# Optimization experiments

Hardware: AMD Instinct MI355X
Metric: run time of the kernel (lower is better)

## Reference

```python
import jax, jax.numpy as jnp
import numpy as np
from math import sqrt

T, B, V = 32, 16, 30000
D, DQKV = 300, 150
K, G = 10, 32            # top-K globals, grapharea_size neighbours each
S = 25000                # last_idx_senses (= SC rows)
EPS = 1e-8


def setup_inputs() -> dict:
    key = jax.random.key(0)
    ks = jax.random.split(key, 6)
    return {
        "predictions_globals": jax.random.normal(ks[0], (T, B, V), jnp.float32),
        "location_context": jax.random.normal(ks[1], (T, B, D), jnp.float32),
        "SC": jax.random.normal(ks[2], (S, D), jnp.float32),
        "Wq": jax.random.normal(ks[3], (D, DQKV), jnp.float32) / sqrt(D),
        "Wk": jax.random.normal(ks[4], (D, DQKV), jnp.float32) / sqrt(D),
        "neighbours_table": jax.random.randint(ks[5], (V, G), 0, S, jnp.int64),
    }


def reference(predictions_globals, location_context, SC, Wq, Wk, neighbours_table):
    # 1) per-sample top-K global selection (sort descending, take K indices)
    _, topk_idx = jax.lax.top_k(predictions_globals, K)          # [T,B,K]
    # 2) sense-neighbour lookup: K globals x G neighbours -> N = K*G senses
    neigh = neighbours_table[topk_idx].reshape(T, B, K * G)      # [T,B,N] int
    # 3) gather precomputed sense contexts
    senses_context = SC[neigh]                                   # [T,B,N,D]
    # 4) ComputeLogits: QK attention logits
    q = location_context @ Wq                                    # [T,B,dqkv]
    k = senses_context @ Wk                                      # [T,B,N,dqkv]
    logits = jnp.einsum("tbd,tbnd->tbn", q, k) / sqrt(DQKV)      # [T,B,N]
    # 5) softmax over neighbours, scatter into full sense distribution
    p = jax.nn.softmax(logits, axis=-1)                          # [T,B,N]
    base = jnp.full((T * B, S), EPS, dtype=p.dtype)
    rows = jnp.arange(T * B)[:, None]                            # [TB,1]
    senses_softmax = base.at[rows, neigh.reshape(T * B, -1)].set(p.reshape(T * B, -1))
    # 6) log-probabilities over all senses
    return jnp.log(senses_softmax)                               # [T*B, S]
```

## Files before the change

kernel.cpp:

```cpp
#include <hip/hip_runtime.h>
#include <math.h>

#define T_ 32
#define B_ 16
#define V_ 30000
#define V4 7500
#define D_ 300
#define DQKV_ 150
#define K_ 10
#define G_ 32
#define N_ 320
#define S_ 25000
#define S4 6250
#define SLICE 3125
#define QKP 304
#define NTS 1024
#define NTP 512
#define NTG 256
#define NTF 384
#define LCAP 4096
#define UTH 0xC0000000u

__device__ __forceinline__ unsigned umap(float f) {
    unsigned b = __float_as_uint(f);
    unsigned mask = (unsigned)(((int)b) >> 31);
    return b ^ (mask | 0x80000000u);
}
__device__ __forceinline__ bool better_u(unsigned au, int ai, unsigned bu, int bi) {
    return (au > bu) || (au == bu && ai < bi);
}

__global__ __launch_bounds__(NTS, 2) void scan_kernel(
    const float* __restrict__ pred, float* __restrict__ out,
    int* __restrict__ wstop)
{
    const int row = blockIdx.x, tid = threadIdx.x;
    const int lane = tid & 63, wave = tid >> 6;
    __shared__ unsigned lu[LCAP];
    __shared__ int      li[LCAP];
    __shared__ int      cnt;

    if (tid == 0) cnt = 0;
    __syncthreads();

    const float FILL = -18.420680743952367f;
    {
        float4 f4 = make_float4(FILL, FILL, FILL, FILL);
        float4* o4 = (float4*)(out + (size_t)row * S_);
        #pragma unroll
        for (int k = 0; k < 7; ++k) { int i = tid + k * NTS; if (i < S4) o4[i] = f4; }
    }

    {
        const float4* p4 = (const float4*)(pred + (size_t)row * V_);
        #pragma unroll
        for (int k = 0; k < 8; ++k) {
            int i = tid + k * NTS;
            if (i < V4) {
                float4 v = p4[i];
                unsigned u0 = umap(v.x), u1 = umap(v.y), u2 = umap(v.z), u3 = umap(v.w);
                int base = i * 4;
                if (u0 >= UTH) { int p = atomicAdd(&cnt, 1); if (p < LCAP) { lu[p] = u0; li[p] = base; } }
                if (u1 >= UTH) { int p = atomicAdd(&cnt, 1); if (p < LCAP) { lu[p] = u1; li[p] = base + 1; } }
                if (u2 >= UTH) { int p = atomicAdd(&cnt, 1); if (p < LCAP) { lu[p] = u2; li[p] = base + 2; } }
                if (u3 >= UTH) { int p = atomicAdd(&cnt, 1); if (p < LCAP) { lu[p] = u3; li[p] = base + 3; } }
            }
        }
    }
    __syncthreads();
    const int c = cnt;

    if (c >= K_ && c <= LCAP) {
        if (wave == 0) {
            for (int p = 0; p < K_; ++p) {
                unsigned bu = 0; int bi = 0x7fffffff;
                for (int s = lane; s < c; s += 64) {
                    unsigned uu = lu[s]; int ii = li[s];
                    if (better_u(uu, ii, bu, bi)) { bu = uu; bi = ii; }
                }
                #pragma unroll
                for (int off = 32; off; off >>= 1) {
                    unsigned ou = __shfl_xor(bu, off, 64);
                    int      oi = __shfl_xor(bi, off, 64);
                    if (better_u(ou, oi, bu, bi)) { bu = ou; bi = oi; }
                }
                if (lane == 0) wstop[row * K_ + p] = bi;
                for (int s = lane; s < c; s += 64)
                    if (li[s] == bi && lu[s] == bu) lu[s] = 0;
            }
        }
    } else {
        if (wave == 0) {
            unsigned tu[K_]; int tix[K_];
            #pragma unroll
            for (int s = 0; s < K_; ++s) { tu[s] = 0; tix[s] = 0x7fffffff; }
            const float* prow = pred + (size_t)row * V_;
            for (int i = lane; i < V_; i += 64) {
                unsigned u = umap(prow[i]);
                if (better_u(u, i, tu[K_-1], tix[K_-1])) {
                    tu[K_-1] = u; tix[K_-1] = i;
                    #pragma unroll
                    for (int s = K_-1; s > 0; --s)
                        if (better_u(tu[s], tix[s], tu[s-1], tix[s-1])) {
                            unsigned a = tu[s]; tu[s] = tu[s-1]; tu[s-1] = a;
                            int b2 = tix[s]; tix[s] = tix[s-1]; tix[s-1] = b2;
                        }
                }
            }
            for (int p = 0; p < K_; ++p) {
                unsigned bu = tu[0]; int bi = tix[0];
                #pragma unroll
                for (int s = 1; s < K_; ++s)
                    if (better_u(tu[s], tix[s], bu, bi)) { bu = tu[s]; bi = tix[s]; }
                #pragma unroll
                for (int off = 32; off; off >>= 1) {
                    unsigned ou = __shfl_xor(bu, off, 64);
                    int      oi = __shfl_xor(bi, off, 64);
                    if (better_u(ou, oi, bu, bi)) { bu = ou; bi = oi; }
                }
                if (lane == 0) wstop[row * K_ + p] = bi;
                #pragma unroll
                for (int s = 0; s < K_; ++s)
                    if (tix[s] == bi) tu[s] = 0;
            }
        }
    }
}

__global__ __launch_bounds__(NTP, 2) void prep_kernel(
    const float* __restrict__ lc, const float* __restrict__ Wq,
    const float* __restrict__ Wk, const int* __restrict__ nbt,
    const int* __restrict__ wstop,
    float* __restrict__ qkws, int* __restrict__ nidxws)
{
    const int row = blockIdx.x, tid = threadIdx.x;
    const int lane = tid & 63, wave = tid >> 6;
    __shared__ int   topg[K_];
    __shared__ __align__(16) float lcs[D_];
    __shared__ float qpart[2][DQKV_];

    if (tid < K_) topg[tid] = wstop[row * K_ + tid];
    if (tid >= 64 && tid < 64 + D_ / 4)
        ((float4*)lcs)[tid - 64] = ((const float4*)(lc + (size_t)row * D_))[tid - 64];
    __syncthreads();

    if (tid < N_) nidxws[(size_t)row * N_ + tid] = nbt[topg[tid >> 5] * G_ + (tid & 31)];

    if (tid < 2 * DQKV_) {
        int h = tid / DQKV_;
        int j = tid - h * DQKV_;
        int d0 = h * 150;
        const float* wp = Wq + (size_t)d0 * DQKV_ + j;
        float a0 = 0.f, a1 = 0.f;
        #pragma unroll 5
        for (int dd = 0; dd < 150; dd += 2) {
            a0 += lcs[d0 + dd]     * wp[(size_t)dd * DQKV_];
            a1 += lcs[d0 + dd + 1] * wp[(size_t)(dd + 1) * DQKV_];
        }
        qpart[h][j] = a0 + a1;
    }
    __syncthreads();

    {
        float qv0 = qpart[0][lane] + qpart[1][lane];
        float qv1 = qpart[0][64 + lane] + qpart[1][64 + lane];
        float qv2 = (lane < 22) ? (qpart[0][128 + lane] + qpart[1][128 + lane]) : 0.f;
        for (int d = wave; d < D_; d += 8) {
            const float* wr = Wk + (size_t)d * DQKV_;
            float w0 = wr[lane];
            float w1 = wr[64 + lane];
            float w2 = (lane < 22) ? wr[128 + lane] : 0.f;
            float p = w0 * qv0 + w1 * qv1 + w2 * qv2;
            #pragma unroll
            for (int off = 32; off; off >>= 1) p += __shfl_xor(p, off, 64);
            if (lane == 0) qkws[(size_t)row * QKP + d] = p;
        }
    }
}

__global__ __launch_bounds__(NTG) void gather_kernel(
    const float* __restrict__ SC, const float* __restrict__ qkws,
    const int* __restrict__ nidxws, float* __restrict__ logws)
{
    const int r = blockIdx.x >> 3;
    const int ch = blockIdx.x & 7;
    const int lo = ch * SLICE, hi = lo + SLICE;
    const int tid = threadIdx.x;
    __shared__ int   nid[N_];
    __shared__ __align__(16) float qk[D_];
    __shared__ int   list[N_];
    __shared__ int   lcnt;

    if (tid == 0) lcnt = 0;
    for (int i = tid; i < N_; i += NTG)
        nid[i] = nidxws[(size_t)r * N_ + i];
    if (tid < D_ / 4)
        ((float4*)qk)[tid] = ((const float4*)(qkws + (size_t)r * QKP))[tid];
    __syncthreads();

    for (int i = tid; i < N_; i += NTG) {
        int sv = nid[i];
        if (sv >= lo && sv < hi) { int p = atomicAdd(&lcnt, 1); list[p] = i; }
    }
    __syncthreads();
    const int c2 = lcnt;

    const float ISC = 0.08164965809277260327f;
    const float4* q4 = (const float4*)qk;
    for (int s = tid; s < 8 * c2; s += NTG) {
        int g = s >> 3, h = s & 7;
        int n = list[g];
        const float4* sc4 = (const float4*)(SC + (size_t)nid[n] * D_);
        int c0 = h * 9;
        float acc = 0.f;
        #pragma unroll
        for (int cc = 0; cc < 9; ++cc) {
            float4 a = sc4[c0 + cc];
            float4 b = q4[c0 + cc];
            acc += a.x * b.x + a.y * b.y + a.z * b.z + a.w * b.w;
        }
        if (h < 3) {
            float4 a = sc4[72 + h];
            float4 b = q4[72 + h];
            acc += a.x * b.x + a.y * b.y + a.z * b.z + a.w * b.w;
        }
        acc += __shfl_xor(acc, 1, 64);
        acc += __shfl_xor(acc, 2, 64);
        acc += __shfl_xor(acc, 4, 64);
        if (h == 0) logws[(size_t)r * N_ + n] = acc * ISC;
    }
}

__global__ __launch_bounds__(NTF) void finalize_kernel(
    const float* __restrict__ logws, const int* __restrict__ nidxws,
    float* __restrict__ out)
{
    const int row = blockIdx.x, tid = threadIdx.x;
    const int lane = tid & 63, wave = tid >> 6;
    __shared__ float lg[N_];
    __shared__ int   nid[N_];
    __shared__ int   kills[N_];
    __shared__ float redA[6], redB[6];
    float* outrow = out + (size_t)row * S_;

    if (tid < N_) {
        lg[tid]  = logws[(size_t)row * N_ + tid];
        nid[tid] = nidxws[(size_t)row * N_ + tid];
        kills[tid] = 0;
    }
    __syncthreads();

    float v = (tid < N_) ? lg[tid] : -INFINITY;
    float m = v;
    #pragma unroll
    for (int off = 32; off; off >>= 1) m = fmaxf(m, __shfl_xor(m, off, 64));
    if (lane == 0) redA[wave] = m;
    __syncthreads();
    m = redA[0];
    #pragma unroll
    for (int w = 1; w < 6; ++w) m = fmaxf(m, redA[w]);

    float ss = (tid < N_) ? expf(v - m) : 0.f;
    #pragma unroll
    for (int off = 32; off; off >>= 1) ss += __shfl_xor(ss, off, 64);
    if (lane == 0) redB[wave] = ss;
    __syncthreads();
    float tot = redB[0];
    #pragma unroll
    for (int w = 1; w < 6; ++w) tot += redB[w];
    float lsum = logf(tot);

    for (int s = tid; s < 4 * N_; s += NTF) {
        int n = s >> 2, cix = s & 3;
        int sidx = nid[n];
        int clo = cix * 80;
        int lo2 = (n + 1 > clo) ? n + 1 : clo;
        int hi2 = clo + 80;
        bool mt = false;
        #pragma unroll 4
        for (int n2 = lo2; n2 < hi2; ++n2) mt |= (nid[n2] == sidx);
        if (mt) kills[n] = 1;
    }
    __syncthreads();

    if (tid < N_ && !kills[tid]) outrow[nid[tid]] = (v - m) - lsum;
}

#define NWS 16
__device__ __forceinline__ bool better(float av, int ai, float bv, int bi) {
    return (av > bv) || (av == bv && ai < bi);
}
__global__ __launch_bounds__(NTS, 4) void selfatt_fused(
    const float* __restrict__ pred, const float* __restrict__ lc,
    const float* __restrict__ SC, const float* __restrict__ Wq,
    const float* __restrict__ Wk, const int* __restrict__ nbt,
    float* __restrict__ out)
{
    const int row = blockIdx.x, tid = threadIdx.x;
    const int lane = tid & 63, wave = tid >> 6;
    __shared__ float wcv[NWS * K_];
    __shared__ int   wci[NWS * K_];
    __shared__ int   topg[K_];
    __shared__ float lcs[D_];
    __shared__ float qs[DQKV_];
    __shared__ __align__(16) float qks[D_];
    __shared__ int   nidx[N_];
    __shared__ float lg[N_];
    __shared__ int   kills[N_];
    __shared__ float redA[NWS], redB[NWS];
    float* outrow = out + (size_t)row * S_;
    const float FILL = -18.420680743952367f;
    {
        float4 f4 = make_float4(FILL, FILL, FILL, FILL);
        float4* o4 = (float4*)outrow;
        #pragma unroll
        for (int k = 0; k < 7; ++k) { int i = tid + k * NTS; if (i < S4) o4[i] = f4; }
    }
    float tv[K_]; int ti[K_];
    #pragma unroll
    for (int s = 0; s < K_; ++s) { tv[s] = -INFINITY; ti[s] = 0x7fffffff; }
    {
        const float4* p4 = (const float4*)(pred + (size_t)row * V_);
        const float4 NEG = make_float4(-INFINITY, -INFINITY, -INFINITY, -INFINITY);
        float4 a[8]; int ib[8];
        #pragma unroll
        for (int u = 0; u < 8; ++u) {
            int i = tid + u * NTS;
            a[u]  = (i < V4) ? p4[i] : NEG;
            ib[u] = (i < V4) ? i * 4 : 0x7ffffff0;
        }
        #pragma unroll
        for (int u = 0; u < 8; ++u) {
            float x = a[u].x, y = a[u].y, z = a[u].z, w = a[u].w;
            float m4 = fmaxf(fmaxf(x, y), fmaxf(z, w));
            if (!(m4 < tv[K_-1])) {
                float vals[4] = {x, y, z, w};
                #pragma unroll
                for (int cc = 0; cc < 4; ++cc) {
                    float val = vals[cc];
                    int   idx = ib[u] + cc;
                    if (better(val, idx, tv[K_-1], ti[K_-1])) {
                        tv[K_-1] = val; ti[K_-1] = idx;
                        #pragma unroll
                        for (int s = K_-1; s > 0; --s) {
                            if (better(tv[s], ti[s], tv[s-1], ti[s-1])) {
                                float fx = tv[s]; tv[s] = tv[s-1]; tv[s-1] = fx;
                                int   iy = ti[s]; ti[s] = ti[s-1]; ti[s-1] = iy;
                            }
                        }
                    }
                }
            }
        }
    }
    for (int p = 0; p < K_; ++p) {
        float bv = tv[0]; int bi = ti[0];
        #pragma unroll
        for (int s = 1; s < K_; ++s)
            if (better(tv[s], ti[s], bv, bi)) { bv = tv[s]; bi = ti[s]; }
        #pragma unroll
        for (int off = 32; off; off >>= 1) {
            float ov = __shfl_xor(bv, off, 64);
            int   oi = __shfl_xor(bi, off, 64);
            if (better(ov, oi, bv, bi)) { bv = ov; bi = oi; }
        }
        if (lane == 0) { wcv[wave * K_ + p] = bv; wci[wave * K_ + p] = bi; }
        #pragma unroll
        for (int s = 0; s < K_; ++s)
            if (ti[s] == bi) tv[s] = -INFINITY;
    }
    __syncthreads();
    if (wave == 0) {
        float c0v = wcv[lane],      c1v = wcv[64 + lane];
        int   c0i = wci[lane],      c1i = wci[64 + lane];
        float c2v = (lane < 32) ? wcv[128 + lane] : -INFINITY;
        int   c2i = (lane < 32) ? wci[128 + lane] : 0x7fffffff;
        for (int p = 0; p < K_; ++p) {
            float bv = c0v; int bi = c0i;
            if (better(c1v, c1i, bv, bi)) { bv = c1v; bi = c1i; }
            if (better(c2v, c2i, bv, bi)) { bv = c2v; bi = c2i; }
            #pragma unroll
            for (int off = 32; off; off >>= 1) {
                float ov = __shfl_xor(bv, off, 64);
                int   oi = __shfl_xor(bi, off, 64);
                if (better(ov, oi, bv, bi)) { bv = ov; bi = oi; }
            }
            if (lane == 0) topg[p] = bi;
            if (c0i == bi) c0v = -INFINITY;
            if (c1i == bi) c1v = -INFINITY;
            if (c2i == bi) c2v = -INFINITY;
        }
    }
    __syncthreads();
    if (tid < N_) { int g = topg[tid >> 5]; nidx[tid] = nbt[g * G_ + (tid & 31)]; }
    else if (tid < 2 * N_) kills[tid - N_] = 0;
    else if (tid >= 640 && tid < 640 + D_) lcs[tid - 640] = lc[(size_t)row * D_ + (tid - 640)];
    __syncthreads();
    if (tid < 600) {
        int j = tid >> 2, h = tid & 3;
        int d0 = h * 75;
        const float* wp = Wq + (size_t)d0 * DQKV_ + j;
        float acc = 0.f;
        #pragma unroll 5
        for (int dd = 0; dd < 75; ++dd) acc += lcs[d0 + dd] * wp[(size_t)dd * DQKV_];
        acc += __shfl_xor(acc, 1, 64);
        acc += __shfl_xor(acc, 2, 64);
        if (h == 0) qs[j] = acc;
    } else {
        int t0 = tid - 600;
        for (int s = t0; s < 4 * N_; s += 424) {
            int n = s >> 2, cc = s & 3;
            int sidx = nidx[n];
            int clo = cc * 80;
            int lo = (n + 1 > clo) ? n + 1 : clo;
            int hi = clo + 80;
            bool mt = false;
            #pragma unroll 4
            for (int n2 = lo; n2 < hi; ++n2) mt |= (nidx[n2] == sidx);
            if (mt) kills[n] = 1;
        }
    }
    __syncthreads();
    if (tid < 600) {
        int d = tid >> 1, h = tid & 1;
        int j0 = h * 75;
        const float* wrow = Wk + (size_t)d * DQKV_ + j0;
        float acc = 0.f;
        #pragma unroll 5
        for (int jj = 0; jj < 75; ++jj) acc += wrow[jj] * qs[j0 + jj];
        acc += __shfl_xor(acc, 1, 64);
        if (h == 0) qks[d] = acc;
    }
    __syncthreads();
    const float ISC = 0.08164965809277260327f;
    const float4* q4 = (const float4*)qks;
    for (int s = tid; s < 8 * N_; s += NTS) {
        int n = s >> 3, h = s & 7;
        const float4* sc4 = (const float4*)(SC + (size_t)nidx[n] * D_);
        int c0 = h * 9;
        float acc = 0.f;
        #pragma unroll
        for (int cc = 0; cc < 9; ++cc) {
            float4 a = sc4[c0 + cc];
            float4 b = q4[c0 + cc];
            acc += a.x * b.x + a.y * b.y + a.z * b.z + a.w * b.w;
        }
        if (h < 3) {
            float4 a = sc4[72 + h];
            float4 b = q4[72 + h];
            acc += a.x * b.x + a.y * b.y + a.z * b.z + a.w * b.w;
        }
        acc += __shfl_xor(acc, 1, 64);
        acc += __shfl_xor(acc, 2, 64);
        acc += __shfl_xor(acc, 4, 64);
        if (h == 0) lg[n] = acc * ISC;
    }
    __syncthreads();
    float v = (tid < N_) ? lg[tid] : -INFINITY;
    float m = v;
    #pragma unroll
    for (int off = 32; off; off >>= 1) m = fmaxf(m, __shfl_xor(m, off, 64));
    if (lane == 0) redA[wave] = m;
    __syncthreads();
    m = redA[0];
    #pragma unroll
    for (int w = 1; w < NWS; ++w) m = fmaxf(m, redA[w]);
    float e = (tid < N_) ? expf(v - m) : 0.f;
    float ss = e;
    #pragma unroll
    for (int off = 32; off; off >>= 1) ss += __shfl_xor(ss, off, 64);
    if (lane == 0) redB[wave] = ss;
    __syncthreads();
    float tot = redB[0];
    #pragma unroll
    for (int w = 1; w < NWS; ++w) tot += redB[w];
    float lsum = logf(tot);
    if (tid < N_ && !kills[tid]) outrow[nidx[tid]] = (v - m) - lsum;
}

extern "C" void kernel_launch(void* const* d_in, const int* in_sizes, int n_in,
                              void* d_out, int out_size, void* d_ws, size_t ws_size,
                              hipStream_t stream) {
    const float* pred = (const float*)d_in[0];
    const float* lc   = (const float*)d_in[1];
    const float* SC   = (const float*)d_in[2];
    const float* Wq   = (const float*)d_in[3];
    const float* Wk   = (const float*)d_in[4];
    const int*   nbt  = (const int*)d_in[5];
    float* out = (float*)d_out;

    const int nrows = T_ * B_;
    const size_t nQK = (size_t)nrows * QKP;
    const size_t nNI = (size_t)nrows * N_;
    const size_t nLG = (size_t)nrows * N_;
    const size_t nTP = (size_t)nrows * K_;
    const size_t need = (nQK + nLG) * sizeof(float) + (nNI + nTP) * sizeof(int);

    if (ws_size >= need) {
        float* qkws   = (float*)d_ws;
        int*   nidxws = (int*)(qkws + nQK);
        float* logws  = (float*)(nidxws + nNI);
        int*   wstop  = (int*)(logws + nLG);
        scan_kernel<<<dim3(nrows), dim3(NTS), 0, stream>>>(pred, out, wstop);
        prep_kernel<<<dim3(nrows), dim3(NTP), 0, stream>>>(
            lc, Wq, Wk, nbt, wstop, qkws, nidxws);
        gather_kernel<<<dim3(nrows * 8), dim3(NTG), 0, stream>>>(
            SC, qkws, nidxws, logws);
        finalize_kernel<<<dim3(nrows), dim3(NTF), 0, stream>>>(
            logws, nidxws, out);
    } else {
        selfatt_fused<<<dim3(T_ * B_), dim3(NTS), 0, stream>>>(
            pred, lc, SC, Wq, Wk, nbt, out);
    }
}
```

Baseline: 110.1 us.

## Merge prep into scan kernel, parallelize top-K selection across waves, recompute neighbour indices

Removes the separate prep kernel. The q·Wk projection now runs in extra blocks of the scan launch, which doubles its grid. The neighbour-index workspace is dropped, and gather and finalize look the indices up directly from the neighbours table using the top-K result. The candidate top-K selection now has all 16 waves compute per-wave top-10 lists from registers, followed by a single-wave merge, replacing one wave scanning the whole shared list ten times. This saves a kernel launch and the serial selection work, at the cost of repeated neighbour-table reads in gather blocks and a per-wave candidate cap of four entries per lane.

```diff
diff --git a/kernel.cpp b/kernel.cpp
--- a/kernel.cpp
+++ b/kernel.cpp
@@ -15,7 +15,6 @@
 #define SLICE 3125
 #define QKP 304
 #define NTS 1024
-#define NTP 512
 #define NTG 256
 #define NTF 384
 #define LCAP 4096
@@ -30,16 +29,59 @@
     return (au > bu) || (au == bu && ai < bi);
 }
 
-__global__ __launch_bounds__(NTS, 2) void scan_kernel(
-    const float* __restrict__ pred, float* __restrict__ out,
-    int* __restrict__ wstop)
+__global__ __launch_bounds__(NTS, 2) void scanqk_kernel(
+    const float* __restrict__ pred, const float* __restrict__ lc,
+    const float* __restrict__ Wq, const float* __restrict__ Wk,
+    float* __restrict__ out, int* __restrict__ wstop, float* __restrict__ qkws)
 {
-    const int row = blockIdx.x, tid = threadIdx.x;
+    const int b = blockIdx.x, tid = threadIdx.x;
     const int lane = tid & 63, wave = tid >> 6;
     __shared__ unsigned lu[LCAP];
     __shared__ int      li[LCAP];
     __shared__ int      cnt;
-
+    __shared__ unsigned wcv[16 * K_];
+    __shared__ int      wci[16 * K_];
+    __shared__ __align__(16) float lcs[D_];
+    __shared__ float    qpart[2][DQKV_];
+
+    if (b >= T_ * B_) {
+        const int row = b - T_ * B_;
+        if (tid < D_ / 4)
+            ((float4*)lcs)[tid] = ((const float4*)(lc + (size_t)row * D_))[tid];
+        __syncthreads();
+
+        if (tid < 2 * DQKV_) {
+            int h = tid / DQKV_;
+            int j = tid - h * DQKV_;
+            int d0 = h * 150;
+            const float* wp = Wq + (size_t)d0 * DQKV_ + j;
+            float a0 = 0.f, a1 = 0.f;
+            #pragma unroll 5
+            for (int dd = 0; dd < 150; dd += 2) {
+                a0 += lcs[d0 + dd]     * wp[(size_t)dd * DQKV_];
+                a1 += lcs[d0 + dd + 1] * wp[(size_t)(dd + 1) * DQKV_];
+            }
+            qpart[h][j] = a0 + a1;
+        }
+        __syncthreads();
+
+        float qv0 = qpart[0][lane] + qpart[1][lane];
+        float qv1 = qpart[0][64 + lane] + qpart[1][64 + lane];
+        float qv2 = (lane < 22) ? (qpart[0][128 + lane] + qpart[1][128 + lane]) : 0.f;
+        for (int d = wave; d < D_; d += 16) {
+            const float* wr = Wk + (size_t)d * DQKV_;
+            float w0 = wr[lane];
+            float w1 = wr[64 + lane];
+            float w2 = (lane < 22) ? wr[128 + lane] : 0.f;
+            float p = w0 * qv0 + w1 * qv1 + w2 * qv2;
+            #pragma unroll
+            for (int off = 32; off; off >>= 1) p += __shfl_xor(p, off, 64);
+            if (lane == 0) qkws[(size_t)row * QKP + d] = p;
+        }
+        return;
+    }
+
+    const int row = b;
     if (tid == 0) cnt = 0;
     __syncthreads();
 
@@ -71,13 +113,41 @@
     const int c = cnt;
 
     if (c >= K_ && c <= LCAP) {
+        unsigned cu[4]; int cix[4];
+        #pragma unroll
+        for (int k = 0; k < 4; ++k) {
+            int s = wave * 64 + lane + k * NTS;
+            bool ok = s < c;
+            cu[k]  = ok ? lu[s] : 0u;
+            cix[k] = ok ? li[s] : 0x7fffffff;
+        }
+        for (int p = 0; p < K_; ++p) {
+            unsigned bu = cu[0]; int bi = cix[0];
+            #pragma unroll
+            for (int k = 1; k < 4; ++k)
+                if (better_u(cu[k], cix[k], bu, bi)) { bu = cu[k]; bi = cix[k]; }
+            #pragma unroll
+            for (int off = 32; off; off >>= 1) {
+                unsigned ou = __shfl_xor(bu, off, 64);
+                int      oi = __shfl_xor(bi, off, 64);
+                if (better_u(ou, oi, bu, bi)) { bu = ou; bi = oi; }
+            }
+            if (lane == 0) { wcv[wave * K_ + p] = bu; wci[wave * K_ + p] = bi; }
+            #pragma unroll
+            for (int k = 0; k < 4; ++k)
+                if (cix[k] == bi) cu[k] = 0u;
+        }
+        __syncthreads();
+
         if (wave == 0) {
+            unsigned c0u = wcv[lane],      c1u = wcv[64 + lane];
+            int      c0i = wci[lane],      c1i = wci[64 + lane];
+            unsigned c2u = (lane < 32) ? wcv[128 + lane] : 0u;
+            int      c2i = (lane < 32) ? wci[128 + lane] : 0x7fffffff;
             for (int p = 0; p < K_; ++p) {
-                unsigned bu = 0; int bi = 0x7fffffff;
-                for (int s = lane; s < c; s += 64) {
-                    unsigned uu = lu[s]; int ii = li[s];
-                    if (better_u(uu, ii, bu, bi)) { bu = uu; bi = ii; }
-                }
+                unsigned bu = c0u; int bi = c0i;
+                if (better_u(c1u, c1i, bu, bi)) { bu = c1u; bi = c1i; }
+                if (better_u(c2u, c2i, bu, bi)) { bu = c2u; bi = c2i; }
                 #pragma unroll
                 for (int off = 32; off; off >>= 1) {
                     unsigned ou = __shfl_xor(bu, off, 64);
@@ -85,8 +155,9 @@
                     if (better_u(ou, oi, bu, bi)) { bu = ou; bi = oi; }
                 }
                 if (lane == 0) wstop[row * K_ + p] = bi;
-                for (int s = lane; s < c; s += 64)
-                    if (li[s] == bi && lu[s] == bu) lu[s] = 0;
+                if (c0i == bi) c0u = 0u;
+                if (c1i == bi) c1u = 0u;
+                if (c2i == bi) c2u = 0u;
             }
         }
     } else {
@@ -127,75 +198,29 @@
     }
 }
 
-__global__ __launch_bounds__(NTP, 2) void prep_kernel(
-    const float* __restrict__ lc, const float* __restrict__ Wq,
-    const float* __restrict__ Wk, const int* __restrict__ nbt,
-    const int* __restrict__ wstop,
-    float* __restrict__ qkws, int* __restrict__ nidxws)
-{
-    const int row = blockIdx.x, tid = threadIdx.x;
-    const int lane = tid & 63, wave = tid >> 6;
-    __shared__ int   topg[K_];
-    __shared__ __align__(16) float lcs[D_];
-    __shared__ float qpart[2][DQKV_];
-
-    if (tid < K_) topg[tid] = wstop[row * K_ + tid];
-    if (tid >= 64 && tid < 64 + D_ / 4)
-        ((float4*)lcs)[tid - 64] = ((const float4*)(lc + (size_t)row * D_))[tid - 64];
-    __syncthreads();
-
-    if (tid < N_) nidxws[(size_t)row * N_ + tid] = nbt[topg[tid >> 5] * G_ + (tid & 31)];
-
-    if (tid < 2 * DQKV_) {
-        int h = tid / DQKV_;
-        int j = tid - h * DQKV_;
-        int d0 = h * 150;
-        const float* wp = Wq + (size_t)d0 * DQKV_ + j;
-        float a0 = 0.f, a1 = 0.f;
-        #pragma unroll 5
-        for (int dd = 0; dd < 150; dd += 2) {
-            a0 += lcs[d0 + dd]     * wp[(size_t)dd * DQKV_];
-            a1 += lcs[d0 + dd + 1] * wp[(size_t)(dd + 1) * DQKV_];
-        }
-        qpart[h][j] = a0 + a1;
-    }
-    __syncthreads();
-
-    {
-        float qv0 = qpart[0][lane] + qpart[1][lane];
-        float qv1 = qpart[0][64 + lane] + qpart[1][64 + lane];
-        float qv2 = (lane < 22) ? (qpart[0][128 + lane] + qpart[1][128 + lane]) : 0.f;
-        for (int d = wave; d < D_; d += 8) {
-            const float* wr = Wk + (size_t)d * DQKV_;
-            float w0 = wr[lane];
-            float w1 = wr[64 + lane];
-            float w2 = (lane < 22) ? wr[128 + lane] : 0.f;
-            float p = w0 * qv0 + w1 * qv1 + w2 * qv2;
-            #pragma unroll
-            for (int off = 32; off; off >>= 1) p += __shfl_xor(p, off, 64);
-            if (lane == 0) qkws[(size_t)row * QKP + d] = p;
-        }
-    }
-}
-
 __global__ __launch_bounds__(NTG) void gather_kernel(
     const float* __restrict__ SC, const float* __restrict__ qkws,
-    const int* __restrict__ nidxws, float* __restrict__ logws)
+    const int* __restrict__ nbt, const int* __restrict__ wstop,
+    float* __restrict__ logws)
 {
     const int r = blockIdx.x >> 3;
     const int ch = blockIdx.x & 7;
     const int lo = ch * SLICE, hi = lo + SLICE;
     const int tid = threadIdx.x;
+    __shared__ int   topg[K_];
     __shared__ int   nid[N_];
     __shared__ __align__(16) float qk[D_];
     __shared__ int   list[N_];
     __shared__ int   lcnt;
 
     if (tid == 0) lcnt = 0;
+    if (tid < K_) topg[tid] = wstop[r * K_ + tid];
+    if (tid >= 64 && tid < 64 + D_ / 4)
+        ((float4*)qk)[tid - 64] = ((const float4*)(qkws + (size_t)r * QKP))[tid - 64];
+    __syncthreads();
+
     for (int i = tid; i < N_; i += NTG)
-        nid[i] = nidxws[(size_t)r * N_ + i];
-    if (tid < D_ / 4)
-        ((float4*)qk)[tid] = ((const float4*)(qkws + (size_t)r * QKP))[tid];
+        nid[i] = nbt[topg[i >> 5] * G_ + (i & 31)];
     __syncthreads();
 
     for (int i = tid; i < N_; i += NTG) {
@@ -216,13 +241,13 @@
         #pragma unroll
         for (int cc = 0; cc < 9; ++cc) {
             float4 a = sc4[c0 + cc];
-            float4 b = q4[c0 + cc];
-            acc += a.x * b.x + a.y * b.y + a.z * b.z + a.w * b.w;
+            float4 bq = q4[c0 + cc];
+            acc += a.x * bq.x + a.y * bq.y + a.z * bq.z + a.w * bq.w;
         }
         if (h < 3) {
             float4 a = sc4[72 + h];
-            float4 b = q4[72 + h];
-            acc += a.x * b.x + a.y * b.y + a.z * b.z + a.w * b.w;
+            float4 bq = q4[72 + h];
+            acc += a.x * bq.x + a.y * bq.y + a.z * bq.z + a.w * bq.w;
         }
         acc += __shfl_xor(acc, 1, 64);
         acc += __shfl_xor(acc, 2, 64);
@@ -232,20 +257,23 @@
 }
 
 __global__ __launch_bounds__(NTF) void finalize_kernel(
-    const float* __restrict__ logws, const int* __restrict__ nidxws,
-    float* __restrict__ out)
+    const float* __restrict__ logws, const int* __restrict__ nbt,
+    const int* __restrict__ wstop, float* __restrict__ out)
 {
     const int row = blockIdx.x, tid = threadIdx.x;
     const int lane = tid & 63, wave = tid >> 6;
+    __shared__ int   topg[K_];
     __shared__ float lg[N_];
     __shared__ int   nid[N_];
     __shared__ int   kills[N_];
     __shared__ float redA[6], redB[6];
     float* outrow = out + (size_t)row * S_;
 
+    if (tid < K_) topg[tid] = wstop[row * K_ + tid];
+    __syncthreads();
     if (tid < N_) {
+        nid[tid] = nbt[topg[tid >> 5] * G_ + (tid & 31)];
         lg[tid]  = logws[(size_t)row * N_ + tid];
-        nid[tid] = nidxws[(size_t)row * N_ + tid];
         kills[tid] = 0;
     }
     __syncthreads();
@@ -491,23 +519,20 @@
 
     const int nrows = T_ * B_;
     const size_t nQK = (size_t)nrows * QKP;
-    const size_t nNI = (size_t)nrows * N_;
     const size_t nLG = (size_t)nrows * N_;
     const size_t nTP = (size_t)nrows * K_;
-    const size_t need = (nQK + nLG) * sizeof(float) + (nNI + nTP) * sizeof(int);
+    const size_t need = (nQK + nLG) * sizeof(float) + nTP * sizeof(int);
 
     if (ws_size >= need) {
-        float* qkws   = (float*)d_ws;
-        int*   nidxws = (int*)(qkws + nQK);
-        float* logws  = (float*)(nidxws + nNI);
-        int*   wstop  = (int*)(logws + nLG);
-        scan_kernel<<<dim3(nrows), dim3(NTS), 0, stream>>>(pred, out, wstop);
-        prep_kernel<<<dim3(nrows), dim3(NTP), 0, stream>>>(
-            lc, Wq, Wk, nbt, wstop, qkws, nidxws);
+        float* qkws  = (float*)d_ws;
+        float* logws = qkws + nQK;
+        int*   wstop = (int*)(logws + nLG);
+        scanqk_kernel<<<dim3(nrows * 2), dim3(NTS), 0, stream>>>(
+            pred, lc, Wq, Wk, out, wstop, qkws);
         gather_kernel<<<dim3(nrows * 8), dim3(NTG), 0, stream>>>(
-            SC, qkws, nidxws, logws);
+            SC, qkws, nbt, wstop, logws);
         finalize_kernel<<<dim3(nrows), dim3(NTF), 0, stream>>>(
-            logws, nidxws, out);
+            logws, nbt, wstop, out);
     } else {
         selfatt_fused<<<dim3(T_ * B_), dim3(NTS), 0, stream>>>(
             pred, lc, SC, Wq, Wk, nbt, out);
```

Result: faster. 101.7 us (-7.6%).
